# Performance work log

Hardware: AMD Instinct MI355X
Metric: run time of the kernel (lower is better)

Reference implementation:

```python
import jax, jax.numpy as jnp
import numpy as np

N_NODES = 50000
N_EDGES = 800000
IN_CH = 128
HID = 128
OUT_CH = 12
NUM_GRAPHS = 512


def _gcn_layer(x, src, dst, W, b, n):
    # GCNConv: out = D^{-1/2} (A + I) D^{-1/2} (x W) + b, messages flow src -> dst
    h = x @ W
    loops = jnp.arange(n)
    s = jnp.concatenate([src, loops])
    d = jnp.concatenate([dst, loops])
    deg = jax.ops.segment_sum(jnp.ones(s.shape[0], dtype=h.dtype), d, num_segments=n)
    dinv = jnp.where(deg > 0, jax.lax.rsqrt(deg), 0.0)
    norm = dinv[s] * dinv[d]                      # [E+N]
    msg = h[s] * norm[:, None]                    # gather + scale
    out = jax.ops.segment_sum(msg, d, num_segments=n)  # scatter-add to targets
    return out + b


def setup_inputs() -> dict:
    key = jax.random.key(0)
    ks = jax.random.split(key, 12)
    x = jax.random.normal(ks[0], (N_NODES, IN_CH), dtype=jnp.float32)
    edge_index = jax.random.randint(ks[1], (2, N_EDGES), 0, N_NODES, dtype=jnp.int64)
    batch = jnp.sort(jax.random.randint(ks[2], (N_NODES,), 0, NUM_GRAPHS, dtype=jnp.int64))
    sc = 0.05
    W0 = jax.random.normal(ks[3], (IN_CH, HID), dtype=jnp.float32) * sc
    b0 = jnp.zeros((HID,), dtype=jnp.float32)
    W1 = jax.random.normal(ks[4], (HID, HID), dtype=jnp.float32) * sc
    b1 = jnp.zeros((HID,), dtype=jnp.float32)
    W2 = jax.random.normal(ks[5], (HID, HID), dtype=jnp.float32) * sc
    b2 = jnp.zeros((HID,), dtype=jnp.float32)
    Wc = jax.random.normal(ks[6], (HID, OUT_CH), dtype=jnp.float32) * sc
    bc = jnp.zeros((OUT_CH,), dtype=jnp.float32)
    return {"x": x, "edge_index": edge_index, "batch": batch,
            "W0": W0, "b0": b0, "W1": W1, "b1": b1, "W2": W2, "b2": b2,
            "Wc": Wc, "bc": bc}


def reference(x, edge_index, batch, W0, b0, W1, b1, W2, b2, Wc, bc):
    src, dst = edge_index[0], edge_index[1]
    n = x.shape[0]
    h = _gcn_layer(x, src, dst, W0, b0, n)
    h = jax.nn.relu(h)  # dropout is identity in eval mode
    h = _gcn_layer(h, src, dst, W1, b1, n)
    h = jax.nn.relu(h)
    h = _gcn_layer(h, src, dst, W2, b2, n)
    # global_mean_pool by graph id
    sums = jax.ops.segment_sum(h, batch, num_segments=NUM_GRAPHS)
    cnt = jax.ops.segment_sum(jnp.ones((n,), dtype=h.dtype), batch, num_segments=NUM_GRAPHS)
    pooled = sums / jnp.maximum(cnt, 1.0)[:, None]
    return pooled @ Wc + bc
```

## Files before the change

### kernel.cpp

```cpp
#include <hip/hip_runtime.h>
#include <hip/hip_bf16.h>


#define CH  128
#define CAP 64
#define NW  8

typedef unsigned int  uint;
typedef unsigned short ushort;
typedef __attribute__((ext_vector_type(8))) short  short8;
typedef __attribute__((ext_vector_type(4))) float  f32x4;
typedef __attribute__((ext_vector_type(4))) int    i32x4;

__device__ inline float bflo(uint u) { return __uint_as_float(u << 16); }
__device__ inline float bfhi(uint u) { return __uint_as_float(u & 0xffff0000u); }
__device__ inline ushort f2bf(float f) {
    uint u = __float_as_uint(f);
    return (ushort)((u + 0x7fffu + ((u >> 16) & 1u)) >> 16);
}

__global__ __launch_bounds__(256) void k_prep0(int4* __restrict__ len4, int nz,
                                               const int* __restrict__ batch,
                                               int* __restrict__ gstart, int n, int G,
                                               const float* __restrict__ W0,
                                               const float* __restrict__ W1,
                                               const float* __restrict__ W2,
                                               ushort* __restrict__ Wt0,
                                               ushort* __restrict__ Wt1,
                                               ushort* __restrict__ Wt2,
                                               int ZB, int BB) {
    int b = blockIdx.x;
    int t = threadIdx.x;
    if (b < ZB) {
        int i = b * 256 + t;
        if (i < nz) len4[i] = make_int4(0, 0, 0, 0);
    } else if (b < ZB + BB) {
        int v = (b - ZB) * 256 + t;
        if (v <= n) {
            int prev = (v == 0) ? -1 : batch[v - 1];
            int cur  = (v == n) ? G  : batch[v];
            for (int g = prev + 1; g <= cur; ++g) gstart[g] = v;
        }
    } else {
        int m = b - ZB - BB;
        const float* W = (m == 0) ? W0 : (m == 1) ? W1 : W2;
        ushort* Wt = (m == 0) ? Wt0 : (m == 1) ? Wt1 : Wt2;
        const float4* wsrc = (const float4*)W;
        #pragma unroll
        for (int i = 0; i < 16; ++i) {
            int c4 = t + i * 256;
            int k  = c4 >> 5;
            int n0 = (c4 & 31) * 4;
            float4 v = wsrc[c4];
            Wt[(n0 + 0) * CH + k] = f2bf(v.x);
            Wt[(n0 + 1) * CH + k] = f2bf(v.y);
            Wt[(n0 + 2) * CH + k] = f2bf(v.z);
            Wt[(n0 + 3) * CH + k] = f2bf(v.w);
        }
    }
}

__global__ __launch_bounds__(256) void k_scatter(const int* __restrict__ src,
                                                 const int* __restrict__ dstv,
                                                 int* __restrict__ len,
                                                 int* __restrict__ csr_src,
                                                 int E, int nper) {
    int p = blockIdx.x & (NW - 1);
    int chunk = blockIdx.x >> 3;
    int lo = p * nper, hi = lo + nper;
    int e0 = (chunk * 256 + threadIdx.x) * 4;
    if (e0 + 3 < E) {
        i32x4 s4 = __builtin_nontemporal_load((const i32x4*)&src[e0]);
        i32x4 d4 = __builtin_nontemporal_load((const i32x4*)&dstv[e0]);
        #pragma unroll
        for (int j = 0; j < 4; ++j) {
            int d = d4[j];
            if (d >= lo && d < hi) {
                int pos = atomicAdd(&len[d], 1);
                if (pos < CAP) csr_src[d * CAP + pos] = s4[j];
            }
        }
    } else {
        for (int e = e0; e < E; ++e) {
            int d = dstv[e];
            if (d >= lo && d < hi) {
                int pos = atomicAdd(&len[d], 1);
                if (pos < CAP) csr_src[d * CAP + pos] = src[e];
            }
        }
    }
}

template<int IN_BF16>
__global__ __launch_bounds__(256) void k_gemm_mfma(const void* __restrict__ Ain,
                                                   const ushort* __restrict__ Wt,
                                                   ushort* __restrict__ C, int M) {
    int tid = threadIdx.x;
    int wid = tid >> 6, lane = tid & 63;
    int row = blockIdx.x * 64 + wid * 16 + (lane & 15);
    int lk  = (lane >> 4) * 8;
    bool rok = row < M;
    f32x4 acc[8] = {};
    #pragma unroll
    for (int ks = 0; ks < 4; ++ks) {
        short8 af = {};
        if (rok) {
            if (IN_BF16) {
                af = *(const short8*)&((const ushort*)Ain)[(size_t)row * CH + ks * 32 + lk];
            } else {
                const float* Af = (const float*)Ain;
                float4 a0 = *(const float4*)&Af[(size_t)row * CH + ks * 32 + lk];
                float4 a1 = *(const float4*)&Af[(size_t)row * CH + ks * 32 + lk + 4];
                af[0] = (short)f2bf(a0.x); af[1] = (short)f2bf(a0.y);
                af[2] = (short)f2bf(a0.z); af[3] = (short)f2bf(a0.w);
                af[4] = (short)f2bf(a1.x); af[5] = (short)f2bf(a1.y);
                af[6] = (short)f2bf(a1.z); af[7] = (short)f2bf(a1.w);
            }
        }
        #pragma unroll
        for (int nt = 0; nt < 8; ++nt) {
            short8 bf = *(const short8*)&Wt[(size_t)(nt * 16 + (lane & 15)) * CH + ks * 32 + lk];
            acc[nt] = __builtin_amdgcn_mfma_f32_16x16x32_bf16(af, bf, acc[nt], 0, 0, 0);
        }
    }
    int ci = (lane >> 4) * 4;
    int cj = lane & 15;
    int rb = blockIdx.x * 64 + wid * 16 + ci;
    #pragma unroll
    for (int nt = 0; nt < 8; ++nt) {
        #pragma unroll
        for (int r = 0; r < 4; ++r) {
            int grow = rb + r;
            if (grow < M) C[(size_t)grow * CH + nt * 16 + cj] = f2bf(acc[nt][r]);
        }
    }
}

template<int OB>
__global__ __launch_bounds__(256) void k_agg(const ushort* __restrict__ T,
                                             const int* __restrict__ len,
                                             const int* __restrict__ csr_src,
                                             const float* __restrict__ bias,
                                             void* __restrict__ outv,
                                             int n, int do_relu) {
    int wid = threadIdx.x >> 6;
    int lane = threadIdx.x & 63;
    int v = blockIdx.x * 4 + wid;
    if (v >= n) return;
    int q = lane >> 4;
    int l16 = lane & 15;
    int c = l16 * 8;
    float acc[8] = {};
    int lv = len[v];
    int beg = v * CAP;
    int end = beg + min(lv, CAP);
    #pragma unroll 2
    for (int p = beg + q; p < end; p += 4) {
        int s = csr_src[p];
        float w = 1.0f / sqrtf((float)(len[s] + 1));
        uint4 row = *(const uint4*)&T[(size_t)s * CH + c];
        acc[0] += w * bflo(row.x); acc[1] += w * bfhi(row.x);
        acc[2] += w * bflo(row.y); acc[3] += w * bfhi(row.y);
        acc[4] += w * bflo(row.z); acc[5] += w * bfhi(row.z);
        acc[6] += w * bflo(row.w); acc[7] += w * bfhi(row.w);
    }
    #pragma unroll
    for (int j = 0; j < 8; ++j) {
        acc[j] += __shfl_xor(acc[j], 16, 64);
        acc[j] += __shfl_xor(acc[j], 32, 64);
    }
    if (q == 0) {
        float di = 1.0f / sqrtf((float)(lv + 1));
        uint4 sv = *(const uint4*)&T[(size_t)v * CH + c];
        float s0 = bflo(sv.x), s1 = bfhi(sv.x), s2 = bflo(sv.y), s3 = bfhi(sv.y);
        float s4 = bflo(sv.z), s5 = bfhi(sv.z), s6 = bflo(sv.w), s7 = bfhi(sv.w);
        float4 ba = *(const float4*)&bias[c];
        float4 bb = *(const float4*)&bias[c + 4];
        float o[8];
        o[0] = (acc[0] + di * s0) * di + ba.x;
        o[1] = (acc[1] + di * s1) * di + ba.y;
        o[2] = (acc[2] + di * s2) * di + ba.z;
        o[3] = (acc[3] + di * s3) * di + ba.w;
        o[4] = (acc[4] + di * s4) * di + bb.x;
        o[5] = (acc[5] + di * s5) * di + bb.y;
        o[6] = (acc[6] + di * s6) * di + bb.z;
        o[7] = (acc[7] + di * s7) * di + bb.w;
        if (do_relu) {
            #pragma unroll
            for (int j = 0; j < 8; ++j) o[j] = fmaxf(o[j], 0.f);
        }
        if (OB) {
            ushort u[8];
            #pragma unroll
            for (int j = 0; j < 8; ++j) u[j] = f2bf(o[j]);
            *(short8*)&((ushort*)outv)[(size_t)v * CH + c] = *(short8*)u;
        } else {
            float* out = (float*)outv;
            *(float4*)&out[(size_t)v * CH + c]     = make_float4(o[0], o[1], o[2], o[3]);
            *(float4*)&out[(size_t)v * CH + c + 4] = make_float4(o[4], o[5], o[6], o[7]);
        }
    }
}

__global__ __launch_bounds__(128) void k_poolcls(const float* __restrict__ h,
                                                 const int* __restrict__ gstart,
                                                 const float* __restrict__ Wc,
                                                 const float* __restrict__ bc,
                                                 float* __restrict__ out, int OUT) {
    __shared__ float p[CH];
    int g = blockIdx.x;
    int t = threadIdx.x;
    int beg = gstart[g], end = gstart[g + 1];
    float acc = 0.f;
    for (int v = beg; v < end; ++v) acc += h[(size_t)v * CH + t];
    float cnt = fmaxf((float)(end - beg), 1.0f);
    p[t] = acc / cnt;
    __syncthreads();
    if (t < OUT) {
        float s = bc[t];
        for (int k = 0; k < CH; ++k) s += p[k] * Wc[k * OUT + t];
        out[g * OUT + t] = s;
    }
}

extern "C" void kernel_launch(void* const* d_in, const int* in_sizes, int n_in,
                              void* d_out, int out_size, void* d_ws, size_t ws_size,
                              hipStream_t stream) {
    const float* x     = (const float*)d_in[0];
    const int*   eidx  = (const int*)d_in[1];
    const int*   batch = (const int*)d_in[2];
    const float* W0 = (const float*)d_in[3];
    const float* b0 = (const float*)d_in[4];
    const float* W1 = (const float*)d_in[5];
    const float* b1 = (const float*)d_in[6];
    const float* W2 = (const float*)d_in[7];
    const float* b2 = (const float*)d_in[8];
    const float* Wc = (const float*)d_in[9];
    const float* bc = (const float*)d_in[10];
    float* out = (float*)d_out;

    const int n = in_sizes[0] / CH;
    const int E = in_sizes[1] / 2;
    const int OUT = 12;
    const int G = out_size / OUT;
    const int* src = eidx;
    const int* dst = eidx + E;

    char* ws = (char*)d_ws;
    size_t off = 0;
    auto carve = [&](size_t bytes) -> char* {
        off = (off + 255) & ~(size_t)255;
        char* p = ws + off;
        off += bytes;
        return p;
    };
    int*    len     = (int*)carve((size_t)n * 4);
    int*    gstart  = (int*)carve((size_t)(G + 1) * 4);
    ushort* Wt0     = (ushort*)carve((size_t)CH * CH * 2);
    ushort* Wt1     = (ushort*)carve((size_t)CH * CH * 2);
    ushort* Wt2     = (ushort*)carve((size_t)CH * CH * 2);
    int*    csr_src = (int*)carve((size_t)n * CAP * 4);
    ushort* T       = (ushort*)carve((size_t)n * CH * 2);
    ushort* bufA    = (ushort*)carve((size_t)n * CH * 2);
    ushort* bufB    = (ushort*)carve((size_t)n * CH * 2);
    float*  bufF    = (float*)carve((size_t)n * CH * 4);
    (void)ws_size;

    const int GB = (n + 63) / 64;
    const int agg_grid = (n + 3) / 4;
    const int nper = (n + NW - 1) / NW;
    const int chunks = (E + 1023) / 1024;
    const int ZB = (n / 4 + 255) / 256;
    const int BB = (n + 1 + 255) / 256;

    k_prep0<<<ZB + BB + 3, 256, 0, stream>>>((int4*)len, n / 4, batch, gstart,
                                             n, G, W0, W1, W2, Wt0, Wt1, Wt2,
                                             ZB, BB);
    k_scatter<<<chunks * NW, 256, 0, stream>>>(src, dst, len, csr_src, E, nper);

    k_gemm_mfma<0><<<GB, 256, 0, stream>>>(x, Wt0, T, n);
    k_agg<1><<<agg_grid, 256, 0, stream>>>(T, len, csr_src, b0, bufA, n, 1);
    k_gemm_mfma<1><<<GB, 256, 0, stream>>>(bufA, Wt1, T, n);
    k_agg<1><<<agg_grid, 256, 0, stream>>>(T, len, csr_src, b1, bufB, n, 1);
    k_gemm_mfma<1><<<GB, 256, 0, stream>>>(bufB, Wt2, T, n);
    k_agg<0><<<agg_grid, 256, 0, stream>>>(T, len, csr_src, b2, bufF, n, 0);

    k_poolcls<<<G, CH, 0, stream>>>(bufF, gstart, Wc, bc, out, OUT);
}
```

Before: 272.0 us.

## Slice features into per-XCD 16-channel planes and store CSR indices as ushort

Feature buffers move from row-major [n][128] to eight channel slices of shape [n][16]. The GEMM writes this layout and the aggregation kernel reads it, and `blockIdx & 7` picks the slice, so round-robin block dispatch should keep each XCD gathering from one slice of about 1.6MB that fits in its L2. The CSR neighbour list is stored as 16-bit indices, which halves index traffic and scatter writes. The trade-off is eight times more, smaller 32-byte gathers per edge, indices that only work for n ≤ 65536, and more shuffle reductions.

```diff
diff --git a/kernel.cpp b/kernel.cpp
--- a/kernel.cpp
+++ b/kernel.cpp
@@ -63,21 +63,20 @@
 __global__ __launch_bounds__(256) void k_scatter(const int* __restrict__ src,
                                                  const int* __restrict__ dstv,
                                                  int* __restrict__ len,
-                                                 int* __restrict__ csr_src,
+                                                 ushort* __restrict__ csr_src,
                                                  int E, int nper) {
     int p = blockIdx.x & (NW - 1);
     int chunk = blockIdx.x >> 3;
     int lo = p * nper, hi = lo + nper;
     int e0 = (chunk * 256 + threadIdx.x) * 4;
     if (e0 + 3 < E) {
-        i32x4 s4 = __builtin_nontemporal_load((const i32x4*)&src[e0]);
         i32x4 d4 = __builtin_nontemporal_load((const i32x4*)&dstv[e0]);
         #pragma unroll
         for (int j = 0; j < 4; ++j) {
             int d = d4[j];
             if (d >= lo && d < hi) {
                 int pos = atomicAdd(&len[d], 1);
-                if (pos < CAP) csr_src[d * CAP + pos] = s4[j];
+                if (pos < CAP) csr_src[d * CAP + pos] = (ushort)src[e0 + j];
             }
         }
     } else {
@@ -85,7 +84,7 @@
             int d = dstv[e];
             if (d >= lo && d < hi) {
                 int pos = atomicAdd(&len[d], 1);
-                if (pos < CAP) csr_src[d * CAP + pos] = src[e];
+                if (pos < CAP) csr_src[d * CAP + pos] = (ushort)src[e];
             }
         }
     }
@@ -106,7 +105,10 @@
         short8 af = {};
         if (rok) {
             if (IN_BF16) {
-                af = *(const short8*)&((const ushort*)Ain)[(size_t)row * CH + ks * 32 + lk];
+                int e = ks * 32 + lk;
+                int sA = e >> 4;
+                int ofs = e & 15;
+                af = *(const short8*)&((const ushort*)Ain)[((size_t)sA * M + row) * 16 + ofs];
             } else {
                 const float* Af = (const float*)Ain;
                 float4 a0 = *(const float4*)&Af[(size_t)row * CH + ks * 32 + lk];
@@ -131,7 +133,7 @@
         #pragma unroll
         for (int r = 0; r < 4; ++r) {
             int grow = rb + r;
-            if (grow < M) C[(size_t)grow * CH + nt * 16 + cj] = f2bf(acc[nt][r]);
+            if (grow < M) C[((size_t)nt * M + grow) * 16 + cj] = f2bf(acc[nt][r]);
         }
     }
 }
@@ -139,26 +141,28 @@
 template<int OB>
 __global__ __launch_bounds__(256) void k_agg(const ushort* __restrict__ T,
                                              const int* __restrict__ len,
-                                             const int* __restrict__ csr_src,
+                                             const ushort* __restrict__ csr,
                                              const float* __restrict__ bias,
                                              void* __restrict__ outv,
                                              int n, int do_relu) {
+    int s = blockIdx.x & (NW - 1);
+    int grp = blockIdx.x >> 3;
     int wid = threadIdx.x >> 6;
     int lane = threadIdx.x & 63;
-    int v = blockIdx.x * 4 + wid;
+    int half = lane >> 5;
+    int l = lane & 31;
+    int pi = l >> 1;
+    int par = l & 1;
+    int v = grp * 8 + wid * 2 + half;
     if (v >= n) return;
-    int q = lane >> 4;
-    int l16 = lane & 15;
-    int c = l16 * 8;
+    const ushort* Ts = T + (size_t)s * n * 16;
+    int lv = len[v];
+    int end = min(lv, CAP);
     float acc[8] = {};
-    int lv = len[v];
-    int beg = v * CAP;
-    int end = beg + min(lv, CAP);
-    #pragma unroll 2
-    for (int p = beg + q; p < end; p += 4) {
-        int s = csr_src[p];
-        float w = 1.0f / sqrtf((float)(len[s] + 1));
-        uint4 row = *(const uint4*)&T[(size_t)s * CH + c];
+    for (int slot = pi; slot < end; slot += 16) {
+        int sidx = csr[v * CAP + slot];
+        float w = 1.0f / sqrtf((float)(len[sidx] + 1));
+        uint4 row = *(const uint4*)&Ts[(size_t)sidx * 16 + par * 8];
         acc[0] += w * bflo(row.x); acc[1] += w * bfhi(row.x);
         acc[2] += w * bflo(row.y); acc[3] += w * bfhi(row.y);
         acc[4] += w * bflo(row.z); acc[5] += w * bfhi(row.z);
@@ -166,25 +170,26 @@
     }
     #pragma unroll
     for (int j = 0; j < 8; ++j) {
+        acc[j] += __shfl_xor(acc[j], 2, 64);
+        acc[j] += __shfl_xor(acc[j], 4, 64);
+        acc[j] += __shfl_xor(acc[j], 8, 64);
         acc[j] += __shfl_xor(acc[j], 16, 64);
-        acc[j] += __shfl_xor(acc[j], 32, 64);
-    }
-    if (q == 0) {
+    }
+    if (l < 2) {
         float di = 1.0f / sqrtf((float)(lv + 1));
-        uint4 sv = *(const uint4*)&T[(size_t)v * CH + c];
-        float s0 = bflo(sv.x), s1 = bfhi(sv.x), s2 = bflo(sv.y), s3 = bfhi(sv.y);
-        float s4 = bflo(sv.z), s5 = bfhi(sv.z), s6 = bflo(sv.w), s7 = bfhi(sv.w);
-        float4 ba = *(const float4*)&bias[c];
-        float4 bb = *(const float4*)&bias[c + 4];
+        uint4 sv = *(const uint4*)&Ts[(size_t)v * 16 + par * 8];
+        float t0 = bflo(sv.x), t1 = bfhi(sv.x), t2 = bflo(sv.y), t3 = bfhi(sv.y);
+        float t4 = bflo(sv.z), t5 = bfhi(sv.z), t6 = bflo(sv.w), t7 = bfhi(sv.w);
+        const float* bs = bias + s * 16 + par * 8;
         float o[8];
-        o[0] = (acc[0] + di * s0) * di + ba.x;
-        o[1] = (acc[1] + di * s1) * di + ba.y;
-        o[2] = (acc[2] + di * s2) * di + ba.z;
-        o[3] = (acc[3] + di * s3) * di + ba.w;
-        o[4] = (acc[4] + di * s4) * di + bb.x;
-        o[5] = (acc[5] + di * s5) * di + bb.y;
-        o[6] = (acc[6] + di * s6) * di + bb.z;
-        o[7] = (acc[7] + di * s7) * di + bb.w;
+        o[0] = (acc[0] + di * t0) * di + bs[0];
+        o[1] = (acc[1] + di * t1) * di + bs[1];
+        o[2] = (acc[2] + di * t2) * di + bs[2];
+        o[3] = (acc[3] + di * t3) * di + bs[3];
+        o[4] = (acc[4] + di * t4) * di + bs[4];
+        o[5] = (acc[5] + di * t5) * di + bs[5];
+        o[6] = (acc[6] + di * t6) * di + bs[6];
+        o[7] = (acc[7] + di * t7) * di + bs[7];
         if (do_relu) {
             #pragma unroll
             for (int j = 0; j < 8; ++j) o[j] = fmaxf(o[j], 0.f);
@@ -193,11 +198,11 @@
             ushort u[8];
             #pragma unroll
             for (int j = 0; j < 8; ++j) u[j] = f2bf(o[j]);
-            *(short8*)&((ushort*)outv)[(size_t)v * CH + c] = *(short8*)u;
+            *(short8*)&((ushort*)outv)[((size_t)s * n + v) * 16 + par * 8] = *(short8*)u;
         } else {
-            float* out = (float*)outv;
-            *(float4*)&out[(size_t)v * CH + c]     = make_float4(o[0], o[1], o[2], o[3]);
-            *(float4*)&out[(size_t)v * CH + c + 4] = make_float4(o[4], o[5], o[6], o[7]);
+            float* of = (float*)outv;
+            *(float4*)&of[((size_t)s * n + v) * 16 + par * 8]     = make_float4(o[0], o[1], o[2], o[3]);
+            *(float4*)&of[((size_t)s * n + v) * 16 + par * 8 + 4] = make_float4(o[4], o[5], o[6], o[7]);
         }
     }
 }
@@ -206,20 +211,22 @@
                                                  const int* __restrict__ gstart,
                                                  const float* __restrict__ Wc,
                                                  const float* __restrict__ bc,
-                                                 float* __restrict__ out, int OUT) {
+                                                 float* __restrict__ out,
+                                                 int n, int OUT) {
     __shared__ float p[CH];
     int g = blockIdx.x;
     int t = threadIdx.x;
+    int s = t >> 4, o = t & 15;
     int beg = gstart[g], end = gstart[g + 1];
     float acc = 0.f;
-    for (int v = beg; v < end; ++v) acc += h[(size_t)v * CH + t];
+    for (int v = beg; v < end; ++v) acc += h[((size_t)s * n + v) * 16 + o];
     float cnt = fmaxf((float)(end - beg), 1.0f);
     p[t] = acc / cnt;
     __syncthreads();
     if (t < OUT) {
-        float s = bc[t];
-        for (int k = 0; k < CH; ++k) s += p[k] * Wc[k * OUT + t];
-        out[g * OUT + t] = s;
+        float sum = bc[t];
+        for (int k = 0; k < CH; ++k) sum += p[(k >> 4) * 16 + (k & 15)] * Wc[k * OUT + t];
+        out[g * OUT + t] = sum;
     }
 }
 
@@ -259,7 +266,7 @@
     ushort* Wt0     = (ushort*)carve((size_t)CH * CH * 2);
     ushort* Wt1     = (ushort*)carve((size_t)CH * CH * 2);
     ushort* Wt2     = (ushort*)carve((size_t)CH * CH * 2);
-    int*    csr_src = (int*)carve((size_t)n * CAP * 4);
+    ushort* csr_src = (ushort*)carve((size_t)n * CAP * 2);
     ushort* T       = (ushort*)carve((size_t)n * CH * 2);
     ushort* bufA    = (ushort*)carve((size_t)n * CH * 2);
     ushort* bufB    = (ushort*)carve((size_t)n * CH * 2);
@@ -267,7 +274,7 @@
     (void)ws_size;
 
     const int GB = (n + 63) / 64;
-    const int agg_grid = (n + 3) / 4;
+    const int agg_grid = NW * ((n + 7) / 8);
     const int nper = (n + NW - 1) / NW;
     const int chunks = (E + 1023) / 1024;
     const int ZB = (n / 4 + 255) / 256;
@@ -285,5 +292,5 @@
     k_gemm_mfma<1><<<GB, 256, 0, stream>>>(bufB, Wt2, T, n);
     k_agg<0><<<agg_grid, 256, 0, stream>>>(T, len, csr_src, b2, bufF, n, 0);
 
-    k_poolcls<<<G, CH, 0, stream>>>(bufF, gstart, Wc, bc, out, OUT);
-}
+    k_poolcls<<<G, CH, 0, stream>>>(bufF, gstart, Wc, bc, out, n, OUT);
+}
```

Measured after the change: 405.0 us. +48.9%, slower.
